# Kernel optimization log

Hardware: AMD Instinct MI355X
Metric: run time of the kernel (lower is better)

Reference implementation:

```python
import jax, jax.numpy as jnp
import numpy as np
from jax import lax

GAMMA = 0.1  # fixed RBF bandwidth from LearnableRBFInfluence


def setup_inputs() -> dict:
    key = jax.random.key(0)
    k1, k2, k3, k4 = jax.random.split(key, 4)
    B, H, W = 2, 256, 256
    NUM_FILTERS, KS, NUM_BASIS = 48, 7, 31
    u_log = jax.random.normal(k1, (B, 1, H, W), jnp.float32)
    f_log = jax.random.normal(k2, (B, 1, H, W), jnp.float32)
    filters = jax.random.normal(k3, (NUM_FILTERS, 1, KS, KS), jnp.float32) * 0.05
    rbf_weights = jax.random.normal(k4, (NUM_FILTERS, NUM_BASIS), jnp.float32) * 0.05
    lambda_param = jnp.float32(0.1)
    return {"u_log": u_log, "f_log": f_log, "filters": filters,
            "rbf_weights": rbf_weights, "lambda_param": lambda_param}


def reference(u_log, f_log, filters, rbf_weights, lambda_param):
    # Batched form of the per-filter loop:
    #   conv[i] = conv2d(u, k_i)  ->  one grouped conv with 48 output channels
    num_basis = rbf_weights.shape[1]
    mu = jnp.linspace(-1.0, 1.0, num_basis).astype(u_log.dtype)  # [K]

    dn = lax.conv_dimension_numbers(u_log.shape, filters.shape, ('NCHW', 'OIHW', 'NCHW'))
    conv = lax.conv_general_dilated(u_log, filters, (1, 1), 'SAME',
                                    dimension_numbers=dn)  # [B,48,H,W]

    # RBF influence, per filter channel c: phi = sum_k w[c,k] * exp(-(conv-mu_k)^2/(2 g^2))
    diff = conv[..., None] - mu                              # [B,48,H,W,K]
    rbf = jnp.exp(-(diff * diff) / (2.0 * GAMMA * GAMMA))
    phi = jnp.einsum('bchwk,ck->bchw', rbf, rbf_weights)     # [B,48,H,W]

    # Per-filter conv2d(phi_i, flip(k_i)) summed over i == single conv
    # with OIHW weight [1,48,7,7] built from spatially-flipped filters.
    kT = jnp.flip(filters, axis=(2, 3)).transpose(1, 0, 2, 3)  # [1,48,7,7]
    dn2 = lax.conv_dimension_numbers(phi.shape, kT.shape, ('NCHW', 'OIHW', 'NCHW'))
    diffusion = lax.conv_general_dilated(phi, kT, (1, 1), 'SAME',
                                         dimension_numbers=dn2)  # [B,1,H,W]

    reaction = lambda_param * (u_log - f_log)
    return u_log - diffusion - reaction
```

## Files before the change

### kernel.cpp

```cpp
#include <hip/hip_runtime.h>

#define HH 256
#define WW 256
#define NPIX (2 * HH * WW)
#define NC 48
#define NB 31
#define NG 6
#define CG 8
#define OT 32
#define PT 38
#define PSTR 44
#define UT 44
#define USTR 52
#define TM 385

__global__ __launch_bounds__(256, 3)
void tnrd_main(const float* __restrict__ u,
               const float* __restrict__ wf,
               const float* __restrict__ wr,
               float* __restrict__ part)
{
    __shared__ __align__(16) float u_s[UT * USTR];
    __shared__ __align__(16) float phi_s[2][PT * PSTR];
    __shared__ __align__(16) float tabs[CG][TM + 1];

    const int tid = threadIdx.x;
    const int bx = blockIdx.x, by = blockIdx.y;
    const int b = blockIdx.z / NG, g = blockIdx.z % NG;
    const int c0 = g * CG;

    const int uy0 = by * OT - 6, ux0 = bx * OT - 6;
    const float* ub = u + b * (HH * WW);
    for (int i = tid; i < UT * USTR; i += 256) {
        int r = i / USTR, c = i - r * USTR;
        int gy = uy0 + r, gx = ux0 + c;
        float v = 0.f;
        if (c < UT && (unsigned)gy < HH && (unsigned)gx < WW)
            v = ub[gy * WW + gx];
        u_s[i] = v;
    }

    #pragma unroll
    for (int ch = 0; ch < CG; ++ch) {
        const float* rc = wr + (c0 + ch) * NB;
        for (int j = tid; j < TM + 1; j += 256) {
            float x = fmaf((float)j, 3.0f / 384.0f, -1.5f);
            float s = 0.f;
            #pragma unroll
            for (int k = 0; k < NB; ++k) {
                float mu = -1.f + (float)k * (1.f / 15.f);
                float d = x - mu;
                s = fmaf(rc[k], __expf(-50.f * d * d), s);
            }
            tabs[ch][j] = s;
        }
    }
    __syncthreads();

    const int oy = tid >> 3;
    const int ox0 = (tid & 7) * 4;
    float o0 = 0.f, o1 = 0.f, o2 = 0.f, o3 = 0.f;
    const int py0 = by * OT - 3, px0 = bx * OT - 3;

    for (int pass = 0; pass < 4; ++pass) {
        const int ca = c0 + 2 * pass;
        const float* wA = wf + ca * 49;
        const float* wB = wA + 49;

        for (int p = 0; p < 2; ++p) {
            const int gi = tid + p * 256;
            if (gi < PT * 10) {
                const int pr = gi / 10, pc = (gi - pr * 10) * 4;
                float a0 = 0.f, a1 = 0.f, a2 = 0.f, a3 = 0.f;
                float b0 = 0.f, b1 = 0.f, b2 = 0.f, b3 = 0.f;
                for (int dy = 0; dy < 7; ++dy) {
                    const float* row = &u_s[(pr + dy) * USTR + pc];
                    float sv[12];
                    #pragma unroll
                    for (int j = 0; j < 12; ++j) sv[j] = row[j];
                    const float* wa = wA + dy * 7;
                    const float* wb = wB + dy * 7;
                    #pragma unroll
                    for (int dx = 0; dx < 7; ++dx) {
                        float fa = wa[dx], fb = wb[dx];
                        a0 = fmaf(sv[dx],     fa, a0);
                        a1 = fmaf(sv[dx + 1], fa, a1);
                        a2 = fmaf(sv[dx + 2], fa, a2);
                        a3 = fmaf(sv[dx + 3], fa, a3);
                        b0 = fmaf(sv[dx],     fb, b0);
                        b1 = fmaf(sv[dx + 1], fb, b1);
                        b2 = fmaf(sv[dx + 2], fb, b2);
                        b3 = fmaf(sv[dx + 3], fb, b3);
                    }
                }
                const int gy = py0 + pr;
                const bool rowok = (unsigned)gy < HH;
                float av[4] = {a0, a1, a2, a3};
                float bv[4] = {b0, b1, b2, b3};
                float pha[4], phb[4];
                #pragma unroll
                for (int j = 0; j < 4; ++j) {
                    bool ok = rowok && (unsigned)(px0 + pc + j) < WW;
                    float ta = fminf(fmaxf(fmaf(av[j], 128.f, 192.f), 0.f), 383.999f);
                    float fja = floorf(ta);
                    float e0a = tabs[2 * 0 + 0][0];
                    (void)e0a;
                    int ia = (int)fja;
                    float va = fmaf(ta - fja, tabs[2*pass][ia+1] - tabs[2*pass][ia],
                                    tabs[2*pass][ia]);
                    float tb = fminf(fmaxf(fmaf(bv[j], 128.f, 192.f), 0.f), 383.999f);
                    float fjb = floorf(tb);
                    int ib = (int)fjb;
                    float vb = fmaf(tb - fjb, tabs[2*pass+1][ib+1] - tabs[2*pass+1][ib],
                                    tabs[2*pass+1][ib]);
                    pha[j] = ok ? va : 0.f;
                    phb[j] = ok ? vb : 0.f;
                }
                float* dA = &phi_s[0][pr * PSTR + pc];
                float* dB = &phi_s[1][pr * PSTR + pc];
                #pragma unroll
                for (int j = 0; j < 4; ++j) dA[j] = pha[j];
                #pragma unroll
                for (int j = 0; j < 4; ++j) dB[j] = phb[j];
            }
        }
        __syncthreads();

        for (int dy = 0; dy < 7; ++dy) {
            const float* rA = &phi_s[0][(oy + dy) * PSTR + ox0];
            const float* rB = &phi_s[1][(oy + dy) * PSTR + ox0];
            float sa[10], sb[10];
            #pragma unroll
            for (int j = 0; j < 10; ++j) sa[j] = rA[j];
            #pragma unroll
            for (int j = 0; j < 10; ++j) sb[j] = rB[j];
            #pragma unroll
            for (int dx = 0; dx < 7; ++dx) {
                float fa = wA[(6 - dy) * 7 + (6 - dx)];
                float fb = wB[(6 - dy) * 7 + (6 - dx)];
                o0 = fmaf(sa[dx],     fa, o0);
                o1 = fmaf(sa[dx + 1], fa, o1);
                o2 = fmaf(sa[dx + 2], fa, o2);
                o3 = fmaf(sa[dx + 3], fa, o3);
                o0 = fmaf(sb[dx],     fb, o0);
                o1 = fmaf(sb[dx + 1], fb, o1);
                o2 = fmaf(sb[dx + 2], fb, o2);
                o3 = fmaf(sb[dx + 3], fb, o3);
            }
        }
        __syncthreads();
    }

    const int gy = by * OT + oy, gx = bx * OT + ox0;
    float4 v4 = make_float4(o0, o1, o2, o3);
    *reinterpret_cast<float4*>(part + (size_t)g * NPIX + b * (HH * WW)
                               + gy * WW + gx) = v4;
}

__global__ __launch_bounds__(256)
void combine_kernel(const float* __restrict__ u,
                    const float* __restrict__ f,
                    const float* __restrict__ lam,
                    const float* __restrict__ part,
                    float* __restrict__ out)
{
    int i = blockIdx.x * 256 + threadIdx.x;
    float d = 0.f;
    #pragma unroll
    for (int g = 0; g < NG; ++g) d += part[g * NPIX + i];
    float lv = lam[0];
    float uv = u[i];
    float fv = f[i];
    out[i] = uv - d - lv * (uv - fv);
}

extern "C" void kernel_launch(void* const* d_in, const int* in_sizes, int n_in,
                              void* d_out, int out_size, void* d_ws, size_t ws_size,
                              hipStream_t stream) {
    const float* u    = (const float*)d_in[0];
    const float* f    = (const float*)d_in[1];
    const float* filt = (const float*)d_in[2];
    const float* rbfw = (const float*)d_in[3];
    const float* lam  = (const float*)d_in[4];
    float* out = (float*)d_out;
    float* part = (float*)d_ws;

    tnrd_main<<<dim3(8, 8, 2 * NG), 256, 0, stream>>>(u, filt, rbfw, part);
    combine_kernel<<<512, 256, 0, stream>>>(u, f, lam, part, out);
}
```

Before: 118.9 us.

## Split channels into more groups, widen phi tile per thread, drop final barrier

```diff
diff --git a/kernel.cpp b/kernel.cpp
--- a/kernel.cpp
+++ b/kernel.cpp
@@ -4,30 +4,36 @@
 #define WW 256
 #define NPIX (2 * HH * WW)
 #define NC 48
-#define NB 31
-#define NG 6
-#define CG 8
 #define OT 32
 #define PT 38
 #define PSTR 44
 #define UT 44
 #define USTR 52
+#define NB 31
 #define TM 385
 
-__global__ __launch_bounds__(256, 3)
+__device__ __forceinline__ float lerp_tab(const float* __restrict__ t, float x) {
+    float s = fminf(fmaxf(fmaf(x, 128.f, 192.f), 0.f), 383.999f);
+    float fj = floorf(s);
+    int i = (int)fj;
+    return fmaf(s - fj, t[i + 1] - t[i], t[i]);
+}
+
+__global__ __launch_bounds__(256, 4)
 void tnrd_main(const float* __restrict__ u,
                const float* __restrict__ wf,
                const float* __restrict__ wr,
-               float* __restrict__ part)
+               float* __restrict__ part,
+               int ng, int cg)
 {
     __shared__ __align__(16) float u_s[UT * USTR];
     __shared__ __align__(16) float phi_s[2][PT * PSTR];
-    __shared__ __align__(16) float tabs[CG][TM + 1];
+    __shared__ __align__(16) float tabs[8][TM + 1];
 
     const int tid = threadIdx.x;
     const int bx = blockIdx.x, by = blockIdx.y;
-    const int b = blockIdx.z / NG, g = blockIdx.z % NG;
-    const int c0 = g * CG;
+    const int b = blockIdx.z / ng, g = blockIdx.z % ng;
+    const int c0 = g * cg;
 
     const int uy0 = by * OT - 6, ux0 = bx * OT - 6;
     const float* ub = u + b * (HH * WW);
@@ -40,8 +46,7 @@
         u_s[i] = v;
     }
 
-    #pragma unroll
-    for (int ch = 0; ch < CG; ++ch) {
+    for (int ch = 0; ch < cg; ++ch) {
         const float* rc = wr + (c0 + ch) * NB;
         for (int j = tid; j < TM + 1; j += 256) {
             float x = fmaf((float)j, 3.0f / 384.0f, -1.5f);
@@ -62,73 +67,71 @@
     float o0 = 0.f, o1 = 0.f, o2 = 0.f, o3 = 0.f;
     const int py0 = by * OT - 3, px0 = bx * OT - 3;
 
-    for (int pass = 0; pass < 4; ++pass) {
-        const int ca = c0 + 2 * pass;
-        const float* wA = wf + ca * 49;
+    const int npass = cg >> 1;
+    for (int pass = 0; pass < npass; ++pass) {
+        const float* wA = wf + (c0 + 2 * pass) * 49;
         const float* wB = wA + 49;
+        const float* tA = tabs[2 * pass];
+        const float* tB = tabs[2 * pass + 1];
 
-        for (int p = 0; p < 2; ++p) {
-            const int gi = tid + p * 256;
-            if (gi < PT * 10) {
-                const int pr = gi / 10, pc = (gi - pr * 10) * 4;
-                float a0 = 0.f, a1 = 0.f, a2 = 0.f, a3 = 0.f;
-                float b0 = 0.f, b1 = 0.f, b2 = 0.f, b3 = 0.f;
-                for (int dy = 0; dy < 7; ++dy) {
-                    const float* row = &u_s[(pr + dy) * USTR + pc];
-                    float sv[12];
-                    #pragma unroll
-                    for (int j = 0; j < 12; ++j) sv[j] = row[j];
-                    const float* wa = wA + dy * 7;
-                    const float* wb = wB + dy * 7;
-                    #pragma unroll
-                    for (int dx = 0; dx < 7; ++dx) {
-                        float fa = wa[dx], fb = wb[dx];
-                        a0 = fmaf(sv[dx],     fa, a0);
-                        a1 = fmaf(sv[dx + 1], fa, a1);
-                        a2 = fmaf(sv[dx + 2], fa, a2);
-                        a3 = fmaf(sv[dx + 3], fa, a3);
-                        b0 = fmaf(sv[dx],     fb, b0);
-                        b1 = fmaf(sv[dx + 1], fb, b1);
-                        b2 = fmaf(sv[dx + 2], fb, b2);
-                        b3 = fmaf(sv[dx + 3], fb, b3);
-                    }
+        if (tid < PT * 5) {
+            const int pr = tid / 5, pc = (tid - pr * 5) * 8;
+            float a0 = 0.f, a1 = 0.f, a2 = 0.f, a3 = 0.f;
+            float a4 = 0.f, a5 = 0.f, a6 = 0.f, a7 = 0.f;
+            float b0 = 0.f, b1 = 0.f, b2 = 0.f, b3 = 0.f;
+            float b4 = 0.f, b5 = 0.f, b6 = 0.f, b7 = 0.f;
+            const float* base = &u_s[pr * USTR + pc];
+            for (int dy = 0; dy < 7; ++dy) {
+                const float* row = base + dy * USTR;
+                float sv[20];
+                #pragma unroll
+                for (int j = 0; j < 20; ++j) sv[j] = row[j];
+                const float* wa = wA + dy * 7;
+                const float* wb = wB + dy * 7;
+                #pragma unroll
+                for (int dx = 0; dx < 7; ++dx) {
+                    const float fa = wa[dx], fb = wb[dx];
+                    a0 = fmaf(sv[dx],     fa, a0);
+                    a1 = fmaf(sv[dx + 1], fa, a1);
+                    a2 = fmaf(sv[dx + 2], fa, a2);
+                    a3 = fmaf(sv[dx + 3], fa, a3);
+                    a4 = fmaf(sv[dx + 4], fa, a4);
+                    a5 = fmaf(sv[dx + 5], fa, a5);
+                    a6 = fmaf(sv[dx + 6], fa, a6);
+                    a7 = fmaf(sv[dx + 7], fa, a7);
+                    b0 = fmaf(sv[dx],     fb, b0);
+                    b1 = fmaf(sv[dx + 1], fb, b1);
+                    b2 = fmaf(sv[dx + 2], fb, b2);
+                    b3 = fmaf(sv[dx + 3], fb, b3);
+                    b4 = fmaf(sv[dx + 4], fb, b4);
+                    b5 = fmaf(sv[dx + 5], fb, b5);
+                    b6 = fmaf(sv[dx + 6], fb, b6);
+                    b7 = fmaf(sv[dx + 7], fb, b7);
                 }
-                const int gy = py0 + pr;
-                const bool rowok = (unsigned)gy < HH;
-                float av[4] = {a0, a1, a2, a3};
-                float bv[4] = {b0, b1, b2, b3};
-                float pha[4], phb[4];
-                #pragma unroll
-                for (int j = 0; j < 4; ++j) {
-                    bool ok = rowok && (unsigned)(px0 + pc + j) < WW;
-                    float ta = fminf(fmaxf(fmaf(av[j], 128.f, 192.f), 0.f), 383.999f);
-                    float fja = floorf(ta);
-                    float e0a = tabs[2 * 0 + 0][0];
-                    (void)e0a;
-                    int ia = (int)fja;
-                    float va = fmaf(ta - fja, tabs[2*pass][ia+1] - tabs[2*pass][ia],
-                                    tabs[2*pass][ia]);
-                    float tb = fminf(fmaxf(fmaf(bv[j], 128.f, 192.f), 0.f), 383.999f);
-                    float fjb = floorf(tb);
-                    int ib = (int)fjb;
-                    float vb = fmaf(tb - fjb, tabs[2*pass+1][ib+1] - tabs[2*pass+1][ib],
-                                    tabs[2*pass+1][ib]);
-                    pha[j] = ok ? va : 0.f;
-                    phb[j] = ok ? vb : 0.f;
-                }
-                float* dA = &phi_s[0][pr * PSTR + pc];
-                float* dB = &phi_s[1][pr * PSTR + pc];
-                #pragma unroll
-                for (int j = 0; j < 4; ++j) dA[j] = pha[j];
-                #pragma unroll
-                for (int j = 0; j < 4; ++j) dB[j] = phb[j];
             }
+            const int gy = py0 + pr;
+            const bool rowok = (unsigned)gy < HH;
+            const float av[8] = {a0, a1, a2, a3, a4, a5, a6, a7};
+            const float bv[8] = {b0, b1, b2, b3, b4, b5, b6, b7};
+            float pa[8], pb[8];
+            #pragma unroll
+            for (int j = 0; j < 8; ++j) {
+                const bool ok = rowok && (unsigned)(px0 + pc + j) < WW;
+                pa[j] = ok ? lerp_tab(tA, av[j]) : 0.f;
+                pb[j] = ok ? lerp_tab(tB, bv[j]) : 0.f;
+            }
+            const int po = pr * PSTR + pc;
+            *(float4*)&phi_s[0][po]     = make_float4(pa[0], pa[1], pa[2], pa[3]);
+            *(float4*)&phi_s[0][po + 4] = make_float4(pa[4], pa[5], pa[6], pa[7]);
+            *(float4*)&phi_s[1][po]     = make_float4(pb[0], pb[1], pb[2], pb[3]);
+            *(float4*)&phi_s[1][po + 4] = make_float4(pb[4], pb[5], pb[6], pb[7]);
         }
         __syncthreads();
 
+        const int co = oy * PSTR + ox0;
         for (int dy = 0; dy < 7; ++dy) {
-            const float* rA = &phi_s[0][(oy + dy) * PSTR + ox0];
-            const float* rB = &phi_s[1][(oy + dy) * PSTR + ox0];
+            const float* rA = &phi_s[0][co + dy * PSTR];
+            const float* rB = &phi_s[1][co + dy * PSTR];
             float sa[10], sb[10];
             #pragma unroll
             for (int j = 0; j < 10; ++j) sa[j] = rA[j];
@@ -136,8 +139,8 @@
             for (int j = 0; j < 10; ++j) sb[j] = rB[j];
             #pragma unroll
             for (int dx = 0; dx < 7; ++dx) {
-                float fa = wA[(6 - dy) * 7 + (6 - dx)];
-                float fb = wB[(6 - dy) * 7 + (6 - dx)];
+                const float fa = wA[(6 - dy) * 7 + (6 - dx)];
+                const float fb = wB[(6 - dy) * 7 + (6 - dx)];
                 o0 = fmaf(sa[dx],     fa, o0);
                 o1 = fmaf(sa[dx + 1], fa, o1);
                 o2 = fmaf(sa[dx + 2], fa, o2);
@@ -148,7 +151,7 @@
                 o3 = fmaf(sb[dx + 3], fb, o3);
             }
         }
-        __syncthreads();
+        if (pass != npass - 1) __syncthreads();
     }
 
     const int gy = by * OT + oy, gx = bx * OT + ox0;
@@ -162,12 +165,11 @@
                     const float* __restrict__ f,
                     const float* __restrict__ lam,
                     const float* __restrict__ part,
-                    float* __restrict__ out)
+                    float* __restrict__ out, int ng)
 {
     int i = blockIdx.x * 256 + threadIdx.x;
     float d = 0.f;
-    #pragma unroll
-    for (int g = 0; g < NG; ++g) d += part[g * NPIX + i];
+    for (int g = 0; g < ng; ++g) d += part[g * NPIX + i];
     float lv = lam[0];
     float uv = u[i];
     float fv = f[i];
@@ -185,6 +187,9 @@
     float* out = (float*)d_out;
     float* part = (float*)d_ws;
 
-    tnrd_main<<<dim3(8, 8, 2 * NG), 256, 0, stream>>>(u, filt, rbfw, part);
-    combine_kernel<<<512, 256, 0, stream>>>(u, f, lam, part, out);
+    const int ng = (ws_size >= (size_t)8 * NPIX * 4) ? 8 : 6;
+    const int cg = NC / ng;
+
+    tnrd_main<<<dim3(8, 8, 2 * ng), 256, 0, stream>>>(u, filt, rbfw, part, ng, cg);
+    combine_kernel<<<512, 256, 0, stream>>>(u, f, lam, part, out, ng);
 }
```

New measurement: 156.1 us. 31.3% more time.
